# Performance work log

Hardware: AMD Instinct MI355X
Metric: run time of the kernel (lower is better)

Reference implementation:

```python
import jax, jax.numpy as jnp
import numpy as np

N, NPG, BS = 32000, 1000, 32
E, H, L, R, K = 512000, 128, 3, 8, 64


def setup_inputs() -> dict:
    key = jax.random.key(0)
    ks = jax.random.split(key, 16)
    sc = 0.05
    x = jax.random.normal(ks[0], (N, H), jnp.float32)
    W_rel = jax.random.normal(ks[1], (L, R, H, H), jnp.float32) * sc
    W_self = jax.random.normal(ks[2], (L, H, H), jnp.float32) * sc
    rel_table = jax.random.normal(ks[3], (R, H), jnp.float32)
    Zn = jax.random.normal(ks[4], (K, H), jnp.float32) * sc
    proj_W = jax.random.normal(ks[5], (L * H, H), jnp.float32) * sc
    proj_b = jnp.zeros((H,), jnp.float32)
    fc_W = jax.random.normal(ks[6], (2 * L * H + 2 * H, 1), jnp.float32) * sc
    fc_b = jnp.zeros((1,), jnp.float32)
    rep_seq = jax.random.normal(ks[7], (BS, H), jnp.float32)
    src = jax.random.randint(ks[8], (E,), 0, N, jnp.int32)
    dst = jax.random.randint(ks[9], (E,), 0, N, jnp.int32)
    etype = jax.random.randint(ks[10], (E,), 0, R, jnp.int32)
    graph_id = (jnp.arange(N, dtype=jnp.int32) // NPG).astype(jnp.int32)
    head_ids = (jnp.arange(BS, dtype=jnp.int32) * NPG)           # node with id==1 per subgraph
    tail_ids = (jnp.arange(BS, dtype=jnp.int32) * NPG + 1)       # node with id==2 per subgraph
    rel_labels = jax.random.randint(ks[11], (BS,), 0, R, jnp.int32)
    return dict(x=x, W_rel=W_rel, W_self=W_self, rel_table=rel_table, Zn=Zn,
                proj_W=proj_W, proj_b=proj_b, fc_W=fc_W, fc_b=fc_b, rep_seq=rep_seq,
                src=src, dst=dst, etype=etype, graph_id=graph_id,
                head_ids=head_ids, tail_ids=tail_ids, rel_labels=rel_labels)


def reference(x, W_rel, W_self, rel_table, Zn, proj_W, proj_b, fc_W, fc_b, rep_seq,
              src, dst, etype, graph_id, head_ids, tail_ids, rel_labels):
    n, h_dim = x.shape
    bs = head_ids.shape[0]
    # RGCN message passing: aggregate src features per (dst, rel), then per-rel linear.
    seg = dst.astype(jnp.int32) * R + etype.astype(jnp.int32)  # [E]
    h = x
    reprs = []
    for l in range(L):
        agg = jax.ops.segment_sum(h[src], seg, num_segments=n * R)  # [N*R, H]
        agg = agg.reshape(n, R, h_dim)
        msg = jnp.einsum('nri,rio->no', agg, W_rel[l])
        h = jax.nn.relu(msg + h @ W_self[l])
        reprs.append(h)
    repr_ = jnp.stack(reprs, axis=1)  # [N, L, H]
    # mean_nodes pooling per subgraph
    counts = jax.ops.segment_sum(jnp.ones((n,), x.dtype), graph_id, num_segments=bs)
    g_mean = jax.ops.segment_sum(repr_, graph_id, num_segments=bs) / counts[:, None, None]
    g_out = jax.nn.leaky_relu(g_mean.reshape(bs, L * h_dim) @ proj_W + proj_b)  # [bs, H]
    # head/tail gathers
    head_flat = repr_[head_ids].reshape(bs, L * h_dim)
    tail_flat = repr_[tail_ids].reshape(bs, L * h_dim)
    rel_embs = rel_table[rel_labels]  # [bs, H]
    h_out = head_flat @ proj_W + proj_b
    t_out = tail_flat @ proj_W + proj_b
    # community view: cluster assignment (softmax) then summary (sigmoid)
    s1 = jax.nn.sigmoid(jax.nn.softmax(h_out @ Zn.T, axis=-1) @ Zn)
    s2 = jax.nn.sigmoid(jax.nn.softmax(t_out @ Zn.T, axis=-1) @ Zn)
    s = s1 * s2
    # view attention aggregation over [subgraph, sequence, community] views
    views = jnp.stack([g_out, rep_seq, s], axis=1)  # [bs, 3, H]
    att = jax.nn.softmax(jnp.sum(rel_embs[:, None, :] * views, axis=-1), axis=-1)  # [bs, 3]
    view_aggr = jnp.sum(att[:, :, None] * views, axis=1)  # [bs, H]
    # positive triplet scoring
    g_rep = jnp.concatenate([head_flat, tail_flat, rel_embs, view_aggr], axis=1)
    out_pos = g_rep @ fc_W + fc_b  # [bs, 1]
    return out_pos
```

## Files before the change

kernel.cpp:

```cpp
#include <hip/hip_runtime.h>

#define N_NODES 32000
#define NPG     1000
#define BSZ     32
#define NEDGE   512000
#define H       128
#define NL      3
#define NR      8

typedef __attribute__((ext_vector_type(8))) short short8;
typedef __attribute__((ext_vector_type(4))) float float4v;

__device__ __forceinline__ float bf2f(unsigned short u) {
  union { unsigned int i; float f; } v;
  v.i = ((unsigned int)u) << 16;
  return v.f;
}
__device__ __forceinline__ unsigned short f2bf(float f) {
  union { float f; unsigned int i; } v;
  v.f = f;
  unsigned int x = v.i;
  return (unsigned short)((x + 0x7FFFu + ((x >> 16) & 1u)) >> 16);
}

__global__ void k_count(const int* __restrict__ dst, int* __restrict__ cnt) {
  int e = blockIdx.x * blockDim.x + threadIdx.x;
  if (e < NEDGE) atomicAdd(&cnt[dst[e]], 1);
}

__global__ void k_scan(int* __restrict__ cursor, int* __restrict__ row_ptr) {
  __shared__ int ssum[256];
  __shared__ int soff[256];
  const int tid = threadIdx.x;
  const int CH = N_NODES / 256;
  const int base = tid * CH;
  int s = 0;
  for (int i = 0; i < CH; ++i) s += cursor[base + i];
  ssum[tid] = s;
  __syncthreads();
  if (tid == 0) {
    int r = 0;
    for (int i = 0; i < 256; ++i) { soff[i] = r; r += ssum[i]; }
    row_ptr[N_NODES] = r;
  }
  __syncthreads();
  int off = soff[tid];
  for (int i = 0; i < CH; ++i) {
    int c = cursor[base + i];
    row_ptr[base + i] = off;
    cursor[base + i] = off;
    off += c;
  }
}

__global__ void k_fill(const int* __restrict__ src, const int* __restrict__ dst,
                       const int* __restrict__ etype, int* __restrict__ cursor,
                       int* __restrict__ edge_dat) {
  int e = blockIdx.x * blockDim.x + threadIdx.x;
  if (e < NEDGE) {
    int p = atomicAdd(&cursor[dst[e]], 1);
    edge_dat[p] = (src[e] << 3) | etype[e];
  }
}

__global__ void k_gcount(const int* __restrict__ graph_id, int* __restrict__ gcount) {
  __shared__ int hist[BSZ];
  const int t = threadIdx.x;
  if (t < BSZ) hist[t] = 0;
  __syncthreads();
  const int n = blockIdx.x * 256 + t;
  if (n < N_NODES) atomicAdd(&hist[graph_id[n]], 1);
  __syncthreads();
  if (t < BSZ) { int v = hist[t]; if (v) atomicAdd(&gcount[t], v); }
}

__global__ void k_cvtX(const float* __restrict__ x, unsigned short* __restrict__ hb) {
  const size_t i = ((size_t)blockIdx.x * blockDim.x + threadIdx.x) * 4;
  float4 v = *(const float4*)(x + i);
  ushort4 u = { f2bf(v.x), f2bf(v.y), f2bf(v.z), f2bf(v.w) };
  *(ushort4*)(hb + i) = u;
}

__global__ void k_cvtB(const float* __restrict__ W_rel, const float* __restrict__ W_self,
                       unsigned short* __restrict__ Bt) {
  const int t = blockIdx.x * blockDim.x + threadIdx.x;
  const int k = t % 1152;
  const int n = (t / 1152) % 128;
  const int l = t / (1152 * 128);
  float v = (k < 1024) ? W_rel[((size_t)l * 1024 + k) * 128 + n]
                       : W_self[((size_t)l * 128 + (k - 1024)) * 128 + n];
  Bt[(size_t)l * (128 * 1152) + (size_t)n * 1152 + k] = f2bf(v);
}

__global__ __launch_bounds__(256) void k_agg(
    const unsigned short* __restrict__ h, const int* __restrict__ row_ptr,
    const int* __restrict__ edge_dat, unsigned short* __restrict__ agg)
{
  const int node = blockIdx.x * 4 + (threadIdx.x >> 6);
  const int lane = threadIdx.x & 63;
  const int c0 = lane * 2;
  float2 a0={0,0},a1={0,0},a2={0,0},a3={0,0},a4={0,0},a5={0,0},a6={0,0},a7={0,0};
  const int beg = row_ptr[node];
  const int end = row_ptr[node + 1];

#define ACC(vv, uu) { \
    float px = bf2f((unsigned short)((uu) & 0xffff)); \
    float py = bf2f((unsigned short)((uu) >> 16)); \
    switch ((vv) & 7) { \
      case 0: a0.x+=px; a0.y+=py; break; case 1: a1.x+=px; a1.y+=py; break; \
      case 2: a2.x+=px; a2.y+=py; break; case 3: a3.x+=px; a3.y+=py; break; \
      case 4: a4.x+=px; a4.y+=py; break; case 5: a5.x+=px; a5.y+=py; break; \
      case 6: a6.x+=px; a6.y+=py; break; case 7: a7.x+=px; a7.y+=py; break; } }

  for (int base = beg; base < end; base += 8) {
    const int cnt = end - base;
    int ed = (lane < 8 && lane < cnt) ? edge_dat[base + lane] : 0;
    if (cnt >= 8) {
      int vv[8]; unsigned int uu[8];
      #pragma unroll
      for (int i = 0; i < 8; ++i) {
        vv[i] = __builtin_amdgcn_readfirstlane(__shfl(ed, i));
        uu[i] = *(const unsigned int*)(h + (size_t)(vv[i] >> 3) * H + c0);
      }
      #pragma unroll
      for (int i = 0; i < 8; ++i) ACC(vv[i], uu[i]);
    } else {
      for (int i = 0; i < cnt; ++i) {
        int v = __builtin_amdgcn_readfirstlane(__shfl(ed, i));
        unsigned int u = *(const unsigned int*)(h + (size_t)(v >> 3) * H + c0);
        ACC(v, u);
      }
    }
  }
#undef ACC

  unsigned short* o = agg + (size_t)node * (NR * H) + c0;
#define ST(r, av) *(unsigned int*)(o + r * H) = (unsigned int)f2bf(av.x) | ((unsigned int)f2bf(av.y) << 16);
  ST(0, a0) ST(1, a1) ST(2, a2) ST(3, a3) ST(4, a4) ST(5, a5) ST(6, a6) ST(7, a7)
#undef ST
}

__global__ __launch_bounds__(256) void k_gemm_mfma(
    const unsigned short* __restrict__ Aagg,
    const unsigned short* __restrict__ Ah,
    const unsigned short* __restrict__ Bt,
    unsigned short* __restrict__ Hnext)
{
  __shared__ unsigned short lds_a[128 * 72];
  __shared__ unsigned short lds_b[128 * 72];
  const int tid  = threadIdx.x;
  const int wave = tid >> 6, lane = tid & 63;
  const int l15 = lane & 15, quad = lane >> 4;
  const int m0 = blockIdx.x * 128;
  const int mb = (wave & 1) * 64;
  const int nb = (wave >> 1) * 64;

  float4v acc[4][4];
  #pragma unroll
  for (int i = 0; i < 4; ++i)
    #pragma unroll
    for (int j = 0; j < 4; ++j) acc[i][j] = (float4v){0.f, 0.f, 0.f, 0.f};

  for (int kc = 0; kc < 1152; kc += 64) {
    __syncthreads();
    const unsigned short* Ap; int lda, kb;
    if (kc < 1024) { Ap = Aagg; lda = 1024; kb = kc; }
    else           { Ap = Ah;   lda = 128;  kb = kc - 1024; }
    #pragma unroll
    for (int s = 0; s < 4; ++s) {
      int f  = s * 256 + tid;
      int m  = f >> 3;
      int ko = (f & 7) * 8;
      *(uint4*)(lds_a + m * 72 + ko) = *(const uint4*)(Ap + (size_t)(m0 + m) * lda + kb + ko);
      *(uint4*)(lds_b + m * 72 + ko) = *(const uint4*)(Bt + (size_t)m * 1152 + kc + ko);
    }
    __syncthreads();
    #pragma unroll
    for (int ks = 0; ks < 2; ++ks) {
      const int ko = ks * 32 + quad * 8;
      short8 afr[4], bfr[4];
      #pragma unroll
      for (int i = 0; i < 4; ++i)
        afr[i] = *(const short8*)(lds_a + (mb + i * 16 + l15) * 72 + ko);
      #pragma unroll
      for (int j = 0; j < 4; ++j)
        bfr[j] = *(const short8*)(lds_b + (nb + j * 16 + l15) * 72 + ko);
      #pragma unroll
      for (int i = 0; i < 4; ++i)
        #pragma unroll
        for (int j = 0; j < 4; ++j)
          acc[i][j] = __builtin_amdgcn_mfma_f32_16x16x32_bf16(afr[i], bfr[j], acc[i][j], 0, 0, 0);
    }
  }
  #pragma unroll
  for (int i = 0; i < 4; ++i)
    #pragma unroll
    for (int j = 0; j < 4; ++j)
      #pragma unroll
      for (int r = 0; r < 4; ++r) {
        int row = m0 + mb + i * 16 + quad * 4 + r;
        int col = nb + j * 16 + l15;
        Hnext[(size_t)row * H + col] = f2bf(fmaxf(acc[i][j][r], 0.f));
      }
}

__global__ void k_gmean(const unsigned short* __restrict__ hb, float* __restrict__ gmean)
{
  const int g = blockIdx.x, l = blockIdx.y, c = blockIdx.z, t = threadIdx.x;
  const unsigned short* base =
      hb + ((size_t)(l + 1) * N_NODES + (size_t)g * NPG + (size_t)c * (NPG / 8)) * H + t * 2;
  float sx = 0.f, sy = 0.f;
  for (int i = 0; i < 125; ++i) {
    unsigned int u = *(const unsigned int*)(base + (size_t)i * H);
    sx += bf2f((unsigned short)(u & 0xffff));
    sy += bf2f((unsigned short)(u >> 16));
  }
  float* gp = gmean + (size_t)g * (NL * H) + l * H + t * 2;
  atomicAdd(gp, sx);
  atomicAdd(gp + 1, sy);
}

__global__ __launch_bounds__(128) void k_final(
    const unsigned short* __restrict__ hb, const float* __restrict__ gmean,
    const int* __restrict__ gcount,
    const float* __restrict__ rel_tb, const float* __restrict__ Zn,
    const float* __restrict__ projW, const float* __restrict__ projB,
    const float* __restrict__ fcW, const float* __restrict__ fcB,
    const float* __restrict__ repSeq,
    const int* __restrict__ head_ids, const int* __restrict__ tail_ids,
    const int* __restrict__ rel_lab, float* __restrict__ out)
{
  const int b = blockIdx.x;
  const int o = threadIdx.x;
  __shared__ float gm[384], hf[384], tf[384];
  __shared__ float go[128], ho[128], t_o[128], re[128], rs[128], sv[128];
  __shared__ float lg[128], pr[128], red[128], att[3];

  const int hid = head_ids[b], tlid = tail_ids[b], rl = rel_lab[b];
  const float cinv = 1.f / (float)gcount[b];
  #pragma unroll
  for (int l = 0; l < NL; ++l) {
    gm[l * H + o] = gmean[(size_t)b * (NL * H) + l * H + o] * cinv;
    hf[l * H + o] = bf2f(hb[((size_t)(l + 1) * N_NODES + hid) * H + o]);
    tf[l * H + o] = bf2f(hb[((size_t)(l + 1) * N_NODES + tlid) * H + o]);
  }
  re[o] = rel_tb[rl * H + o];
  rs[o] = repSeq[b * H + o];
  __syncthreads();

  float pb = projB[o];
  float sg = pb, sh = pb, st = pb;
  for (int i = 0; i < NL * H; ++i) {
    float wv = projW[i * H + o];
    sg = fmaf(gm[i], wv, sg);
    sh = fmaf(hf[i], wv, sh);
    st = fmaf(tf[i], wv, st);
  }
  go[o] = (sg > 0.f) ? sg : 0.01f * sg;
  ho[o] = sh;
  t_o[o] = st;
  __syncthreads();

  {
    const int k = o & 63;
    const float* v = (o < 64) ? ho : t_o;
    float s = 0.f;
    for (int i = 0; i < H; ++i) s = fmaf(v[i], Zn[k * H + i], s);
    lg[o] = s;
  }
  __syncthreads();
  if (o < 2) {
    float* l0 = &lg[o * 64];
    float* p0 = &pr[o * 64];
    float mx = l0[0];
    for (int k = 1; k < 64; ++k) mx = fmaxf(mx, l0[k]);
    float sum = 0.f;
    for (int k = 0; k < 64; ++k) { float e = __expf(l0[k] - mx); p0[k] = e; sum += e; }
    float inv = 1.f / sum;
    for (int k = 0; k < 64; ++k) p0[k] *= inv;
  }
  __syncthreads();
  {
    float s1 = 0.f, s2 = 0.f;
    for (int k = 0; k < 64; ++k) {
      float z = Zn[k * H + o];
      s1 = fmaf(pr[k], z, s1);
      s2 = fmaf(pr[64 + k], z, s2);
    }
    s1 = 1.f / (1.f + __expf(-s1));
    s2 = 1.f / (1.f + __expf(-s2));
    sv[o] = s1 * s2;
  }
  __syncthreads();
  if (o == 0) {
    float d0 = 0.f, d1 = 0.f, d2 = 0.f;
    for (int i = 0; i < H; ++i) { d0 += re[i] * go[i]; d1 += re[i] * rs[i]; d2 += re[i] * sv[i]; }
    float mx = fmaxf(d0, fmaxf(d1, d2));
    float e0 = __expf(d0 - mx), e1 = __expf(d1 - mx), e2 = __expf(d2 - mx);
    float inv = 1.f / (e0 + e1 + e2);
    att[0] = e0 * inv; att[1] = e1 * inv; att[2] = e2 * inv;
  }
  __syncthreads();
  float va = att[0] * go[o] + att[1] * rs[o] + att[2] * sv[o];

  float p = 0.f;
  p = fmaf(hf[o],       fcW[o],       p);
  p = fmaf(hf[128 + o], fcW[128 + o], p);
  p = fmaf(hf[256 + o], fcW[256 + o], p);
  p = fmaf(tf[o],       fcW[384 + o], p);
  p = fmaf(tf[128 + o], fcW[512 + o], p);
  p = fmaf(tf[256 + o], fcW[640 + o], p);
  p = fmaf(re[o],       fcW[768 + o], p);
  p = fmaf(va,          fcW[896 + o], p);
  red[o] = p;
  __syncthreads();
  if (o == 0) {
    float s = 0.f;
    for (int i = 0; i < 128; ++i) s += red[i];
    out[b] = s + fcB[0];
  }
}

extern "C" void kernel_launch(void* const* d_in, const int* in_sizes, int n_in,
                              void* d_out, int out_size, void* d_ws, size_t ws_size,
                              hipStream_t stream) {
  const float* x        = (const float*)d_in[0];
  const float* W_rel    = (const float*)d_in[1];
  const float* W_self   = (const float*)d_in[2];
  const float* rel_tb   = (const float*)d_in[3];
  const float* Zn       = (const float*)d_in[4];
  const float* proj_W   = (const float*)d_in[5];
  const float* proj_b   = (const float*)d_in[6];
  const float* fc_W     = (const float*)d_in[7];
  const float* fc_b     = (const float*)d_in[8];
  const float* rep_seq  = (const float*)d_in[9];
  const int* src      = (const int*)d_in[10];
  const int* dst      = (const int*)d_in[11];
  const int* etype    = (const int*)d_in[12];
  const int* graph_id = (const int*)d_in[13];
  const int* head_ids = (const int*)d_in[14];
  const int* tail_ids = (const int*)d_in[15];
  const int* rel_lab  = (const int*)d_in[16];
  float* out = (float*)d_out;

  char* w = (char*)d_ws;
  unsigned short* agg_bf = (unsigned short*)w; w += (size_t)N_NODES * 1024 * 2;
  unsigned short* hb     = (unsigned short*)w; w += (size_t)(NL + 1) * N_NODES * H * 2;
  unsigned short* Bt = (unsigned short*)w; w += (size_t)NL * 128 * 1152 * 2;
  int* row_ptr = (int*)w;   w += (size_t)32004 * 4;
  int* edge_dat= (int*)w;   w += (size_t)NEDGE * 4;
  char* z = w;
  int* cursor  = (int*)w;   w += (size_t)N_NODES * 4;
  int* gcount  = (int*)w;   w += (size_t)32 * 4;
  float* gmean = (float*)w; w += (size_t)BSZ * NL * H * 4;
  size_t zbytes = (size_t)(w - z);

  hipMemsetAsync(z, 0, zbytes, stream);
  k_count <<<NEDGE / 256, 256, 0, stream>>>(dst, cursor);
  k_scan  <<<1, 256, 0, stream>>>(cursor, row_ptr);
  k_fill  <<<NEDGE / 256, 256, 0, stream>>>(src, dst, etype, cursor, edge_dat);
  k_gcount<<<(N_NODES + 255) / 256, 256, 0, stream>>>(graph_id, gcount);
  k_cvtX  <<<(N_NODES * H) / (256 * 4), 256, 0, stream>>>(x, hb);
  k_cvtB  <<<(NL * 128 * 1152) / 256, 256, 0, stream>>>(W_rel, W_self, Bt);

  for (int l = 0; l < NL; ++l) {
    const unsigned short* hp = hb + (size_t)l * N_NODES * H;
    unsigned short* hn = hb + (size_t)(l + 1) * N_NODES * H;
    k_agg <<<N_NODES / 4, 256, 0, stream>>>(hp, row_ptr, edge_dat, agg_bf);
    k_gemm_mfma<<<N_NODES / 128, 256, 0, stream>>>(
        agg_bf, hp, Bt + (size_t)l * 128 * 1152, hn);
  }
  k_gmean<<<dim3(BSZ, NL, 8), 64, 0, stream>>>(hb, gmean);
  k_final<<<BSZ, H, 0, stream>>>(hb, gmean, gcount, rel_tb, Zn, proj_W, proj_b, fc_W, fc_b,
                                 rep_seq, head_ids, tail_ids, rel_lab, out);
  (void)in_sizes; (void)n_in; (void)out_size; (void)ws_size;
}
```

Measured before the change: 395.9 us.

## Transform node features per relation before gathering instead of aggregating first

Reorders the RGCN layer so each node's features are first multiplied by all 8 relation weights plus the self weight in one dense MFMA GEMM (N x 1152 output). A gather kernel then sums the pre-transformed rows for each edge using precomputed offsets, adds the self term and applies ReLU. This removes the 8-way per-relation accumulator switch and the large K=1152 GEMM over the aggregated buffer. In exchange it writes a 9x wider intermediate, and the gather now reads rows spread over a larger array. Messages are now rounded to bf16 before summation, which changes numerics slightly.

```diff
diff --git a/kernel.cpp b/kernel.cpp
--- a/kernel.cpp
+++ b/kernel.cpp
@@ -7,6 +7,7 @@
 #define H       128
 #define NL      3
 #define NR      8
+#define NW      1152
 
 typedef __attribute__((ext_vector_type(8))) short short8;
 typedef __attribute__((ext_vector_type(4))) float float4v;
@@ -55,11 +56,11 @@
 
 __global__ void k_fill(const int* __restrict__ src, const int* __restrict__ dst,
                        const int* __restrict__ etype, int* __restrict__ cursor,
-                       int* __restrict__ edge_dat) {
+                       int* __restrict__ edge_off) {
   int e = blockIdx.x * blockDim.x + threadIdx.x;
   if (e < NEDGE) {
     int p = atomicAdd(&cursor[dst[e]], 1);
-    edge_dat[p] = (src[e] << 3) | etype[e];
+    edge_off[p] = src[e] * NW + etype[e] * H;
   }
 }
 
@@ -84,124 +85,119 @@
 __global__ void k_cvtB(const float* __restrict__ W_rel, const float* __restrict__ W_self,
                        unsigned short* __restrict__ Bt) {
   const int t = blockIdx.x * blockDim.x + threadIdx.x;
-  const int k = t % 1152;
-  const int n = (t / 1152) % 128;
-  const int l = t / (1152 * 128);
-  float v = (k < 1024) ? W_rel[((size_t)l * 1024 + k) * 128 + n]
-                       : W_self[((size_t)l * 128 + (k - 1024)) * 128 + n];
-  Bt[(size_t)l * (128 * 1152) + (size_t)n * 1152 + k] = f2bf(v);
-}
-
-__global__ __launch_bounds__(256) void k_agg(
-    const unsigned short* __restrict__ h, const int* __restrict__ row_ptr,
-    const int* __restrict__ edge_dat, unsigned short* __restrict__ agg)
+  const int k = t & 127;
+  const int n = (t >> 7) % NW;
+  const int l = t / (NW * H);
+  float v = (n < 1024) ? W_rel[(((size_t)l * NR + (n >> 7)) * H + k) * H + (n & 127)]
+                       : W_self[((size_t)l * H + k) * H + (n - 1024)];
+  Bt[(size_t)l * (NW * H) + (size_t)n * H + k] = f2bf(v);
+}
+
+__global__ __launch_bounds__(256) void k_gemm9(
+    const unsigned short* __restrict__ Ah,
+    const unsigned short* __restrict__ Bt,
+    unsigned short* __restrict__ G)
+{
+  __shared__ unsigned short lds_a[128 * 136];
+  __shared__ unsigned short lds_b[128 * 136];
+  const int tid  = threadIdx.x;
+  const int wave = tid >> 6, lane = tid & 63;
+  const int l15 = lane & 15, quad = lane >> 4;
+  const int m0 = blockIdx.x * 128;
+  const int n0 = blockIdx.y * 128;
+  const int mb = (wave & 1) * 64;
+  const int nb = (wave >> 1) * 64;
+
+  #pragma unroll
+  for (int s = 0; s < 8; ++s) {
+    int f  = s * 256 + tid;
+    int m  = f >> 4;
+    int ko = (f & 15) * 8;
+    *(uint4*)(lds_a + m * 136 + ko) = *(const uint4*)(Ah + (size_t)(m0 + m) * H + ko);
+    *(uint4*)(lds_b + m * 136 + ko) = *(const uint4*)(Bt + (size_t)(n0 + m) * H + ko);
+  }
+  __syncthreads();
+
+  float4v acc[4][4];
+  #pragma unroll
+  for (int i = 0; i < 4; ++i)
+    #pragma unroll
+    for (int j = 0; j < 4; ++j) acc[i][j] = (float4v){0.f, 0.f, 0.f, 0.f};
+
+  #pragma unroll
+  for (int ks = 0; ks < 4; ++ks) {
+    const int ko = ks * 32 + quad * 8;
+    short8 afr[4], bfr[4];
+    #pragma unroll
+    for (int i = 0; i < 4; ++i)
+      afr[i] = *(const short8*)(lds_a + (mb + i * 16 + l15) * 136 + ko);
+    #pragma unroll
+    for (int j = 0; j < 4; ++j)
+      bfr[j] = *(const short8*)(lds_b + (nb + j * 16 + l15) * 136 + ko);
+    #pragma unroll
+    for (int i = 0; i < 4; ++i)
+      #pragma unroll
+      for (int j = 0; j < 4; ++j)
+        acc[i][j] = __builtin_amdgcn_mfma_f32_16x16x32_bf16(afr[i], bfr[j], acc[i][j], 0, 0, 0);
+  }
+
+  __syncthreads();
+  #pragma unroll
+  for (int i = 0; i < 4; ++i)
+    #pragma unroll
+    for (int j = 0; j < 4; ++j)
+      #pragma unroll
+      for (int r = 0; r < 4; ++r)
+        lds_a[(mb + i * 16 + quad * 4 + r) * 136 + nb + j * 16 + l15] = f2bf(acc[i][j][r]);
+  __syncthreads();
+  #pragma unroll
+  for (int s = 0; s < 8; ++s) {
+    int f  = s * 256 + tid;
+    int m  = f >> 4;
+    int ko = (f & 15) * 8;
+    *(uint4*)(G + (size_t)(m0 + m) * NW + n0 + ko) = *(const uint4*)(lds_a + m * 136 + ko);
+  }
+}
+
+__global__ __launch_bounds__(256) void k_gather(
+    const unsigned short* __restrict__ G, const int* __restrict__ row_ptr,
+    const int* __restrict__ edge_off, unsigned short* __restrict__ Hnext)
 {
   const int node = blockIdx.x * 4 + (threadIdx.x >> 6);
   const int lane = threadIdx.x & 63;
   const int c0 = lane * 2;
-  float2 a0={0,0},a1={0,0},a2={0,0},a3={0,0},a4={0,0},a5={0,0},a6={0,0},a7={0,0};
   const int beg = row_ptr[node];
   const int end = row_ptr[node + 1];
-
-#define ACC(vv, uu) { \
-    float px = bf2f((unsigned short)((uu) & 0xffff)); \
-    float py = bf2f((unsigned short)((uu) >> 16)); \
-    switch ((vv) & 7) { \
-      case 0: a0.x+=px; a0.y+=py; break; case 1: a1.x+=px; a1.y+=py; break; \
-      case 2: a2.x+=px; a2.y+=py; break; case 3: a3.x+=px; a3.y+=py; break; \
-      case 4: a4.x+=px; a4.y+=py; break; case 5: a5.x+=px; a5.y+=py; break; \
-      case 6: a6.x+=px; a6.y+=py; break; case 7: a7.x+=px; a7.y+=py; break; } }
-
-  for (int base = beg; base < end; base += 8) {
-    const int cnt = end - base;
-    int ed = (lane < 8 && lane < cnt) ? edge_dat[base + lane] : 0;
-    if (cnt >= 8) {
-      int vv[8]; unsigned int uu[8];
-      #pragma unroll
-      for (int i = 0; i < 8; ++i) {
-        vv[i] = __builtin_amdgcn_readfirstlane(__shfl(ed, i));
-        uu[i] = *(const unsigned int*)(h + (size_t)(vv[i] >> 3) * H + c0);
-      }
-      #pragma unroll
-      for (int i = 0; i < 8; ++i) ACC(vv[i], uu[i]);
-    } else {
-      for (int i = 0; i < cnt; ++i) {
-        int v = __builtin_amdgcn_readfirstlane(__shfl(ed, i));
-        unsigned int u = *(const unsigned int*)(h + (size_t)(v >> 3) * H + c0);
-        ACC(v, u);
-      }
+  float sx, sy;
+  {
+    unsigned int u = *(const unsigned int*)(G + (size_t)node * NW + 1024 + c0);
+    sx = bf2f((unsigned short)(u & 0xffff));
+    sy = bf2f((unsigned short)(u >> 16));
+  }
+  int e = beg;
+  for (; e + 8 <= end; e += 8) {
+    int of[8]; unsigned int u[8];
+    #pragma unroll
+    for (int i = 0; i < 8; ++i) of[i] = edge_off[e + i];
+    #pragma unroll
+    for (int i = 0; i < 8; ++i)
+      u[i] = *(const unsigned int*)(G + (size_t)of[i] + c0);
+    #pragma unroll
+    for (int i = 0; i < 8; ++i) {
+      sx += bf2f((unsigned short)(u[i] & 0xffff));
+      sy += bf2f((unsigned short)(u[i] >> 16));
     }
   }
-#undef ACC
-
-  unsigned short* o = agg + (size_t)node * (NR * H) + c0;
-#define ST(r, av) *(unsigned int*)(o + r * H) = (unsigned int)f2bf(av.x) | ((unsigned int)f2bf(av.y) << 16);
-  ST(0, a0) ST(1, a1) ST(2, a2) ST(3, a3) ST(4, a4) ST(5, a5) ST(6, a6) ST(7, a7)
-#undef ST
-}
-
-__global__ __launch_bounds__(256) void k_gemm_mfma(
-    const unsigned short* __restrict__ Aagg,
-    const unsigned short* __restrict__ Ah,
-    const unsigned short* __restrict__ Bt,
-    unsigned short* __restrict__ Hnext)
-{
-  __shared__ unsigned short lds_a[128 * 72];
-  __shared__ unsigned short lds_b[128 * 72];
-  const int tid  = threadIdx.x;
-  const int wave = tid >> 6, lane = tid & 63;
-  const int l15 = lane & 15, quad = lane >> 4;
-  const int m0 = blockIdx.x * 128;
-  const int mb = (wave & 1) * 64;
-  const int nb = (wave >> 1) * 64;
-
-  float4v acc[4][4];
-  #pragma unroll
-  for (int i = 0; i < 4; ++i)
-    #pragma unroll
-    for (int j = 0; j < 4; ++j) acc[i][j] = (float4v){0.f, 0.f, 0.f, 0.f};
-
-  for (int kc = 0; kc < 1152; kc += 64) {
-    __syncthreads();
-    const unsigned short* Ap; int lda, kb;
-    if (kc < 1024) { Ap = Aagg; lda = 1024; kb = kc; }
-    else           { Ap = Ah;   lda = 128;  kb = kc - 1024; }
-    #pragma unroll
-    for (int s = 0; s < 4; ++s) {
-      int f  = s * 256 + tid;
-      int m  = f >> 3;
-      int ko = (f & 7) * 8;
-      *(uint4*)(lds_a + m * 72 + ko) = *(const uint4*)(Ap + (size_t)(m0 + m) * lda + kb + ko);
-      *(uint4*)(lds_b + m * 72 + ko) = *(const uint4*)(Bt + (size_t)m * 1152 + kc + ko);
-    }
-    __syncthreads();
-    #pragma unroll
-    for (int ks = 0; ks < 2; ++ks) {
-      const int ko = ks * 32 + quad * 8;
-      short8 afr[4], bfr[4];
-      #pragma unroll
-      for (int i = 0; i < 4; ++i)
-        afr[i] = *(const short8*)(lds_a + (mb + i * 16 + l15) * 72 + ko);
-      #pragma unroll
-      for (int j = 0; j < 4; ++j)
-        bfr[j] = *(const short8*)(lds_b + (nb + j * 16 + l15) * 72 + ko);
-      #pragma unroll
-      for (int i = 0; i < 4; ++i)
-        #pragma unroll
-        for (int j = 0; j < 4; ++j)
-          acc[i][j] = __builtin_amdgcn_mfma_f32_16x16x32_bf16(afr[i], bfr[j], acc[i][j], 0, 0, 0);
-    }
-  }
-  #pragma unroll
-  for (int i = 0; i < 4; ++i)
-    #pragma unroll
-    for (int j = 0; j < 4; ++j)
-      #pragma unroll
-      for (int r = 0; r < 4; ++r) {
-        int row = m0 + mb + i * 16 + quad * 4 + r;
-        int col = nb + j * 16 + l15;
-        Hnext[(size_t)row * H + col] = f2bf(fmaxf(acc[i][j][r], 0.f));
-      }
+  for (; e < end; ++e) {
+    int of = edge_off[e];
+    unsigned int u = *(const unsigned int*)(G + (size_t)of + c0);
+    sx += bf2f((unsigned short)(u & 0xffff));
+    sy += bf2f((unsigned short)(u >> 16));
+  }
+  sx = fmaxf(sx, 0.f);
+  sy = fmaxf(sy, 0.f);
+  *(unsigned int*)(Hnext + (size_t)node * H + c0) =
+      (unsigned int)f2bf(sx) | ((unsigned int)f2bf(sy) << 16);
 }
 
 __global__ void k_gmean(const unsigned short* __restrict__ hb, float* __restrict__ gmean)
@@ -344,11 +340,11 @@
   float* out = (float*)d_out;
 
   char* w = (char*)d_ws;
-  unsigned short* agg_bf = (unsigned short*)w; w += (size_t)N_NODES * 1024 * 2;
-  unsigned short* hb     = (unsigned short*)w; w += (size_t)(NL + 1) * N_NODES * H * 2;
-  unsigned short* Bt = (unsigned short*)w; w += (size_t)NL * 128 * 1152 * 2;
-  int* row_ptr = (int*)w;   w += (size_t)32004 * 4;
-  int* edge_dat= (int*)w;   w += (size_t)NEDGE * 4;
+  unsigned short* G  = (unsigned short*)w; w += (size_t)N_NODES * NW * 2;
+  unsigned short* hb = (unsigned short*)w; w += (size_t)(NL + 1) * N_NODES * H * 2;
+  unsigned short* Bt = (unsigned short*)w; w += (size_t)NL * NW * H * 2;
+  int* row_ptr  = (int*)w;  w += (size_t)32004 * 4;
+  int* edge_off = (int*)w;  w += (size_t)NEDGE * 4;
   char* z = w;
   int* cursor  = (int*)w;   w += (size_t)N_NODES * 4;
   int* gcount  = (int*)w;   w += (size_t)32 * 4;
@@ -358,17 +354,16 @@
   hipMemsetAsync(z, 0, zbytes, stream);
   k_count <<<NEDGE / 256, 256, 0, stream>>>(dst, cursor);
   k_scan  <<<1, 256, 0, stream>>>(cursor, row_ptr);
-  k_fill  <<<NEDGE / 256, 256, 0, stream>>>(src, dst, etype, cursor, edge_dat);
+  k_fill  <<<NEDGE / 256, 256, 0, stream>>>(src, dst, etype, cursor, edge_off);
   k_gcount<<<(N_NODES + 255) / 256, 256, 0, stream>>>(graph_id, gcount);
   k_cvtX  <<<(N_NODES * H) / (256 * 4), 256, 0, stream>>>(x, hb);
-  k_cvtB  <<<(NL * 128 * 1152) / 256, 256, 0, stream>>>(W_rel, W_self, Bt);
+  k_cvtB  <<<(NL * NW * H) / 256, 256, 0, stream>>>(W_rel, W_self, Bt);
 
   for (int l = 0; l < NL; ++l) {
     const unsigned short* hp = hb + (size_t)l * N_NODES * H;
     unsigned short* hn = hb + (size_t)(l + 1) * N_NODES * H;
-    k_agg <<<N_NODES / 4, 256, 0, stream>>>(hp, row_ptr, edge_dat, agg_bf);
-    k_gemm_mfma<<<N_NODES / 128, 256, 0, stream>>>(
-        agg_bf, hp, Bt + (size_t)l * 128 * 1152, hn);
+    k_gemm9 <<<dim3(N_NODES / 128, 9), 256, 0, stream>>>(hp, Bt + (size_t)l * NW * H, G);
+    k_gather<<<N_NODES / 4, 256, 0, stream>>>(G, row_ptr, edge_off, hn);
   }
   k_gmean<<<dim3(BSZ, NL, 8), 64, 0, stream>>>(hb, gmean);
   k_final<<<BSZ, H, 0, stream>>>(hb, gmean, gcount, rel_tb, Zn, proj_W, proj_b, fc_W, fc_b,
```

Measured after the change: 384.9 us. -2.8%, faster.

## Sort edges by (dst, relation) segment and fuse preprocessing kernels

Applied to the files above, without the earlier changes.

Builds the CSR over dst*R+etype segments instead of dst nodes, so each wave aggregates a single segment without the per-edge relation switch. Edge data now holds a precomputed element offset (src<<7). The single-block scan becomes a three-stage parallel scan over 256K segments, and the count, convert and graph-count kernels are merged into one block-partitioned prep kernel to cut launches. In exchange the aggregation grid is 8x larger, with many tiny segments of about two edges each, and more row-pointer reads.

```diff
diff --git a/kernel.cpp b/kernel.cpp
--- a/kernel.cpp
+++ b/kernel.cpp
@@ -7,6 +7,7 @@
 #define H       128
 #define NL      3
 #define NR      8
+#define NSEG    (N_NODES * NR)
 
 typedef __attribute__((ext_vector_type(8))) short short8;
 typedef __attribute__((ext_vector_type(4))) float float4v;
@@ -23,34 +24,92 @@
   return (unsigned short)((x + 0x7FFFu + ((x >> 16) & 1u)) >> 16);
 }
 
-__global__ void k_count(const int* __restrict__ dst, int* __restrict__ cnt) {
-  int e = blockIdx.x * blockDim.x + threadIdx.x;
-  if (e < NEDGE) atomicAdd(&cnt[dst[e]], 1);
-}
-
-__global__ void k_scan(int* __restrict__ cursor, int* __restrict__ row_ptr) {
-  __shared__ int ssum[256];
-  __shared__ int soff[256];
-  const int tid = threadIdx.x;
-  const int CH = N_NODES / 256;
-  const int base = tid * CH;
-  int s = 0;
-  for (int i = 0; i < CH; ++i) s += cursor[base + i];
-  ssum[tid] = s;
-  __syncthreads();
-  if (tid == 0) {
+__global__ __launch_bounds__(256) void k_prep(
+    const float* __restrict__ x, const float* __restrict__ W_rel,
+    const float* __restrict__ W_self, const int* __restrict__ dst,
+    const int* __restrict__ etype, const int* __restrict__ graph_id,
+    unsigned short* __restrict__ hb, unsigned short* __restrict__ Bt,
+    int* __restrict__ cnt, int* __restrict__ gcount)
+{
+  const int b = blockIdx.x, t = threadIdx.x;
+  if (b < 4000) {
+    const size_t i = ((size_t)b * 256 + t) * 4;
+    float4 v = *(const float4*)(x + i);
+    ushort4 u = { f2bf(v.x), f2bf(v.y), f2bf(v.z), f2bf(v.w) };
+    *(ushort4*)(hb + i) = u;
+  } else if (b < 5728) {
+    const int g = (b - 4000) * 256 + t;
+    const int k = g % 1152;
+    const int n = (g / 1152) % 128;
+    const int l = g / (1152 * 128);
+    float v = (k < 1024) ? W_rel[((size_t)l * 1024 + k) * 128 + n]
+                         : W_self[((size_t)l * 128 + (k - 1024)) * 128 + n];
+    Bt[(size_t)l * (128 * 1152) + (size_t)n * 1152 + k] = f2bf(v);
+  } else if (b < 7728) {
+    const int e = (b - 5728) * 256 + t;
+    atomicAdd(&cnt[dst[e] * NR + etype[e]], 1);
+  } else {
+    __shared__ int hist[BSZ];
+    if (t < BSZ) hist[t] = 0;
+    __syncthreads();
+    const int n = (b - 7728) * 256 + t;
+    if (n < N_NODES) atomicAdd(&hist[graph_id[n]], 1);
+    __syncthreads();
+    if (t < BSZ) { int v = hist[t]; if (v) atomicAdd(&gcount[t], v); }
+  }
+}
+
+__global__ __launch_bounds__(256) void k_scanA(const int* __restrict__ cnt,
+                                               int* __restrict__ bsum) {
+  __shared__ int red[256];
+  const int t = threadIdx.x;
+  int4 v = *(const int4*)(cnt + blockIdx.x * 1024 + t * 4);
+  red[t] = v.x + v.y + v.z + v.w;
+  __syncthreads();
+  for (int off = 128; off > 0; off >>= 1) {
+    if (t < off) red[t] += red[t + off];
+    __syncthreads();
+  }
+  if (t == 0) bsum[blockIdx.x] = red[0];
+}
+
+__global__ __launch_bounds__(256) void k_scanB(const int* __restrict__ bsum,
+                                               int* __restrict__ boff,
+                                               int* __restrict__ row_ptr2) {
+  __shared__ int v[256];
+  const int t = threadIdx.x;
+  v[t] = (t < 250) ? bsum[t] : 0;
+  __syncthreads();
+  if (t == 0) {
     int r = 0;
-    for (int i = 0; i < 256; ++i) { soff[i] = r; r += ssum[i]; }
-    row_ptr[N_NODES] = r;
-  }
-  __syncthreads();
-  int off = soff[tid];
-  for (int i = 0; i < CH; ++i) {
-    int c = cursor[base + i];
-    row_ptr[base + i] = off;
-    cursor[base + i] = off;
-    off += c;
-  }
+    for (int i = 0; i < 250; ++i) { int c = v[i]; v[i] = r; r += c; }
+    row_ptr2[NSEG] = r;
+  }
+  __syncthreads();
+  if (t < 250) boff[t] = v[t];
+}
+
+__global__ __launch_bounds__(256) void k_scanC(const int* __restrict__ cnt,
+                                               const int* __restrict__ boff,
+                                               int* __restrict__ row_ptr2,
+                                               int* __restrict__ cursor) {
+  __shared__ int ts[256];
+  const int t = threadIdx.x;
+  const int base = blockIdx.x * 1024 + t * 4;
+  int4 v = *(const int4*)(cnt + base);
+  const int s = v.x + v.y + v.z + v.w;
+  ts[t] = s;
+  __syncthreads();
+  for (int off = 1; off < 256; off <<= 1) {
+    int val = (t >= off) ? ts[t - off] : 0;
+    __syncthreads();
+    ts[t] += val;
+    __syncthreads();
+  }
+  int ex = ts[t] - s + boff[blockIdx.x];
+  int4 w = { ex, ex + v.x, ex + v.x + v.y, ex + v.x + v.y + v.z };
+  *(int4*)(row_ptr2 + base) = w;
+  *(int4*)(cursor + base) = w;
 }
 
 __global__ void k_fill(const int* __restrict__ src, const int* __restrict__ dst,
@@ -58,86 +117,41 @@
                        int* __restrict__ edge_dat) {
   int e = blockIdx.x * blockDim.x + threadIdx.x;
   if (e < NEDGE) {
-    int p = atomicAdd(&cursor[dst[e]], 1);
-    edge_dat[p] = (src[e] << 3) | etype[e];
-  }
-}
-
-__global__ void k_gcount(const int* __restrict__ graph_id, int* __restrict__ gcount) {
-  __shared__ int hist[BSZ];
-  const int t = threadIdx.x;
-  if (t < BSZ) hist[t] = 0;
-  __syncthreads();
-  const int n = blockIdx.x * 256 + t;
-  if (n < N_NODES) atomicAdd(&hist[graph_id[n]], 1);
-  __syncthreads();
-  if (t < BSZ) { int v = hist[t]; if (v) atomicAdd(&gcount[t], v); }
-}
-
-__global__ void k_cvtX(const float* __restrict__ x, unsigned short* __restrict__ hb) {
-  const size_t i = ((size_t)blockIdx.x * blockDim.x + threadIdx.x) * 4;
-  float4 v = *(const float4*)(x + i);
-  ushort4 u = { f2bf(v.x), f2bf(v.y), f2bf(v.z), f2bf(v.w) };
-  *(ushort4*)(hb + i) = u;
-}
-
-__global__ void k_cvtB(const float* __restrict__ W_rel, const float* __restrict__ W_self,
-                       unsigned short* __restrict__ Bt) {
-  const int t = blockIdx.x * blockDim.x + threadIdx.x;
-  const int k = t % 1152;
-  const int n = (t / 1152) % 128;
-  const int l = t / (1152 * 128);
-  float v = (k < 1024) ? W_rel[((size_t)l * 1024 + k) * 128 + n]
-                       : W_self[((size_t)l * 128 + (k - 1024)) * 128 + n];
-  Bt[(size_t)l * (128 * 1152) + (size_t)n * 1152 + k] = f2bf(v);
+    int p = atomicAdd(&cursor[dst[e] * NR + etype[e]], 1);
+    edge_dat[p] = src[e] << 7;
+  }
 }
 
 __global__ __launch_bounds__(256) void k_agg(
-    const unsigned short* __restrict__ h, const int* __restrict__ row_ptr,
+    const unsigned short* __restrict__ h, const int* __restrict__ row_ptr2,
     const int* __restrict__ edge_dat, unsigned short* __restrict__ agg)
 {
-  const int node = blockIdx.x * 4 + (threadIdx.x >> 6);
+  const int seg = blockIdx.x * 4 + (threadIdx.x >> 6);
   const int lane = threadIdx.x & 63;
   const int c0 = lane * 2;
-  float2 a0={0,0},a1={0,0},a2={0,0},a3={0,0},a4={0,0},a5={0,0},a6={0,0},a7={0,0};
-  const int beg = row_ptr[node];
-  const int end = row_ptr[node + 1];
-
-#define ACC(vv, uu) { \
-    float px = bf2f((unsigned short)((uu) & 0xffff)); \
-    float py = bf2f((unsigned short)((uu) >> 16)); \
-    switch ((vv) & 7) { \
-      case 0: a0.x+=px; a0.y+=py; break; case 1: a1.x+=px; a1.y+=py; break; \
-      case 2: a2.x+=px; a2.y+=py; break; case 3: a3.x+=px; a3.y+=py; break; \
-      case 4: a4.x+=px; a4.y+=py; break; case 5: a5.x+=px; a5.y+=py; break; \
-      case 6: a6.x+=px; a6.y+=py; break; case 7: a7.x+=px; a7.y+=py; break; } }
-
-  for (int base = beg; base < end; base += 8) {
-    const int cnt = end - base;
-    int ed = (lane < 8 && lane < cnt) ? edge_dat[base + lane] : 0;
-    if (cnt >= 8) {
-      int vv[8]; unsigned int uu[8];
-      #pragma unroll
-      for (int i = 0; i < 8; ++i) {
-        vv[i] = __builtin_amdgcn_readfirstlane(__shfl(ed, i));
-        uu[i] = *(const unsigned int*)(h + (size_t)(vv[i] >> 3) * H + c0);
-      }
-      #pragma unroll
-      for (int i = 0; i < 8; ++i) ACC(vv[i], uu[i]);
-    } else {
-      for (int i = 0; i < cnt; ++i) {
-        int v = __builtin_amdgcn_readfirstlane(__shfl(ed, i));
-        unsigned int u = *(const unsigned int*)(h + (size_t)(v >> 3) * H + c0);
-        ACC(v, u);
-      }
-    }
-  }
-#undef ACC
-
-  unsigned short* o = agg + (size_t)node * (NR * H) + c0;
-#define ST(r, av) *(unsigned int*)(o + r * H) = (unsigned int)f2bf(av.x) | ((unsigned int)f2bf(av.y) << 16);
-  ST(0, a0) ST(1, a1) ST(2, a2) ST(3, a3) ST(4, a4) ST(5, a5) ST(6, a6) ST(7, a7)
-#undef ST
+  const int beg = row_ptr2[seg];
+  const int end = row_ptr2[seg + 1];
+  float sx = 0.f, sy = 0.f;
+  int e = beg;
+  for (; e + 4 <= end; e += 4) {
+    int o0 = edge_dat[e], o1 = edge_dat[e + 1], o2 = edge_dat[e + 2], o3 = edge_dat[e + 3];
+    unsigned int u0 = *(const unsigned int*)(h + o0 + c0);
+    unsigned int u1 = *(const unsigned int*)(h + o1 + c0);
+    unsigned int u2 = *(const unsigned int*)(h + o2 + c0);
+    unsigned int u3 = *(const unsigned int*)(h + o3 + c0);
+    sx += bf2f((unsigned short)(u0 & 0xffff)) + bf2f((unsigned short)(u1 & 0xffff))
+        + bf2f((unsigned short)(u2 & 0xffff)) + bf2f((unsigned short)(u3 & 0xffff));
+    sy += bf2f((unsigned short)(u0 >> 16)) + bf2f((unsigned short)(u1 >> 16))
+        + bf2f((unsigned short)(u2 >> 16)) + bf2f((unsigned short)(u3 >> 16));
+  }
+  for (; e < end; ++e) {
+    int o = edge_dat[e];
+    unsigned int u = *(const unsigned int*)(h + o + c0);
+    sx += bf2f((unsigned short)(u & 0xffff));
+    sy += bf2f((unsigned short)(u >> 16));
+  }
+  *(unsigned int*)(agg + (size_t)seg * H + c0) =
+      (unsigned int)f2bf(sx) | ((unsigned int)f2bf(sy) << 16);
 }
 
 __global__ __launch_bounds__(256) void k_gemm_mfma(
@@ -344,31 +358,32 @@
   float* out = (float*)d_out;
 
   char* w = (char*)d_ws;
-  unsigned short* agg_bf = (unsigned short*)w; w += (size_t)N_NODES * 1024 * 2;
-  unsigned short* hb     = (unsigned short*)w; w += (size_t)(NL + 1) * N_NODES * H * 2;
-  unsigned short* Bt = (unsigned short*)w; w += (size_t)NL * 128 * 1152 * 2;
-  int* row_ptr = (int*)w;   w += (size_t)32004 * 4;
-  int* edge_dat= (int*)w;   w += (size_t)NEDGE * 4;
+  unsigned short* agg = (unsigned short*)w; w += (size_t)NSEG * H * 2;
+  unsigned short* hb  = (unsigned short*)w; w += (size_t)(NL + 1) * N_NODES * H * 2;
+  unsigned short* Bt  = (unsigned short*)w; w += (size_t)NL * 128 * 1152 * 2;
+  int* row_ptr2 = (int*)w;  w += (size_t)(NSEG + 4) * 4;
+  int* edge_dat = (int*)w;  w += (size_t)NEDGE * 4;
+  int* bsum     = (int*)w;  w += (size_t)256 * 4;
+  int* boff     = (int*)w;  w += (size_t)256 * 4;
   char* z = w;
-  int* cursor  = (int*)w;   w += (size_t)N_NODES * 4;
+  int* cursor  = (int*)w;   w += (size_t)NSEG * 4;
   int* gcount  = (int*)w;   w += (size_t)32 * 4;
   float* gmean = (float*)w; w += (size_t)BSZ * NL * H * 4;
   size_t zbytes = (size_t)(w - z);
 
   hipMemsetAsync(z, 0, zbytes, stream);
-  k_count <<<NEDGE / 256, 256, 0, stream>>>(dst, cursor);
-  k_scan  <<<1, 256, 0, stream>>>(cursor, row_ptr);
-  k_fill  <<<NEDGE / 256, 256, 0, stream>>>(src, dst, etype, cursor, edge_dat);
-  k_gcount<<<(N_NODES + 255) / 256, 256, 0, stream>>>(graph_id, gcount);
-  k_cvtX  <<<(N_NODES * H) / (256 * 4), 256, 0, stream>>>(x, hb);
-  k_cvtB  <<<(NL * 128 * 1152) / 256, 256, 0, stream>>>(W_rel, W_self, Bt);
+  k_prep <<<7853, 256, 0, stream>>>(x, W_rel, W_self, dst, etype, graph_id,
+                                    hb, Bt, cursor, gcount);
+  k_scanA<<<NSEG / 1024, 256, 0, stream>>>(cursor, bsum);
+  k_scanB<<<1, 256, 0, stream>>>(bsum, boff, row_ptr2);
+  k_scanC<<<NSEG / 1024, 256, 0, stream>>>(cursor, boff, row_ptr2, cursor);
+  k_fill <<<NEDGE / 256, 256, 0, stream>>>(src, dst, etype, cursor, edge_dat);
 
   for (int l = 0; l < NL; ++l) {
     const unsigned short* hp = hb + (size_t)l * N_NODES * H;
     unsigned short* hn = hb + (size_t)(l + 1) * N_NODES * H;
-    k_agg <<<N_NODES / 4, 256, 0, stream>>>(hp, row_ptr, edge_dat, agg_bf);
-    k_gemm_mfma<<<N_NODES / 128, 256, 0, stream>>>(
-        agg_bf, hp, Bt + (size_t)l * 128 * 1152, hn);
+    k_agg <<<NSEG / 4, 256, 0, stream>>>(hp, row_ptr2, edge_dat, agg);
+    k_gemm_mfma<<<N_NODES / 128, 256, 0, stream>>>(agg, hp, Bt + (size_t)l * 128 * 1152, hn);
   }
   k_gmean<<<dim3(BSZ, NL, 8), 64, 0, stream>>>(hb, gmean);
   k_final<<<BSZ, H, 0, stream>>>(hb, gmean, gcount, rel_tb, Zn, proj_W, proj_b, fc_W, fc_b,
```

Measured after the change: 449.5 us. 13.6% more time.
